# Kernel tuning notes

Hardware: AMD Instinct MI355X
Metric: run time of the kernel (lower is better)

Reference implementation:

```python
import jax, jax.numpy as jnp
import numpy as np

C = 256
CK = C // 8  # query/key projection dim

def conv1x1(x, w, b):
    # x: (B,C,H,W), w: (O,C), b: (O,)
    return jnp.einsum('bchw,oc->bohw', x, w) + b[None, :, None, None]

def conv3x3(x, w, b):
    # w: (O,C,3,3)
    y = jax.lax.conv_general_dilated(x, w, window_strides=(1, 1), padding='SAME',
                                     dimension_numbers=('NCHW', 'OIHW', 'NCHW'))
    return y + b[None, :, None, None]

def setup_inputs() -> dict:
    key = jax.random.key(0)
    ks = jax.random.split(key, 24)
    s = 0.05
    d = {
        'x1': jax.random.normal(ks[0], (4, C, 64, 64), jnp.float32),
        'x2': jax.random.normal(ks[1], (4, C, 64, 64), jnp.float32),
        'wq1': jax.random.normal(ks[2], (CK, C), jnp.float32) * s,
        'bq1': jax.random.normal(ks[3], (CK,), jnp.float32) * s,
        'wk1': jax.random.normal(ks[4], (CK, C), jnp.float32) * s,
        'bk1': jax.random.normal(ks[5], (CK,), jnp.float32) * s,
        'wv1': jax.random.normal(ks[6], (C, C), jnp.float32) * s,
        'bv1': jax.random.normal(ks[7], (C,), jnp.float32) * s,
        'wq2': jax.random.normal(ks[8], (CK, C), jnp.float32) * s,
        'bq2': jax.random.normal(ks[9], (CK,), jnp.float32) * s,
        'wk2': jax.random.normal(ks[10], (CK, C), jnp.float32) * s,
        'bk2': jax.random.normal(ks[11], (CK,), jnp.float32) * s,
        'wv2': jax.random.normal(ks[12], (C, C), jnp.float32) * s,
        'bv2': jax.random.normal(ks[13], (C,), jnp.float32) * s,
        'wd1': jax.random.normal(ks[14], (C, C), jnp.float32) * s,
        'bd1': jax.random.normal(ks[15], (C,), jnp.float32) * s,
        'wd3': jax.random.normal(ks[16], (C, C, 3, 3), jnp.float32) * s,
        'bd3': jax.random.normal(ks[17], (C,), jnp.float32) * s,
        'gamma1': jax.random.normal(ks[18], (1,), jnp.float32) * 0.5,
        'gamma2': jax.random.normal(ks[19], (1,), jnp.float32) * 0.5,
    }
    return d

def reference(x1, x2, wq1, bq1, wk1, bk1, wv1, bv1, wq2, bq2, wk2, bk2, wv2, bv2,
              wd1, bd1, wd3, bd3, gamma1, gamma2):
    B, Cc, H, W = x1.shape
    N = H * W
    # projections (1x1 convs), flattened to (B, d, N)
    q1 = conv1x1(x1, wq1, bq1).reshape(B, CK, N)
    k1 = conv1x1(x1, wk1, bk1).reshape(B, CK, N)
    v1 = conv1x1(x1, wv1, bv1).reshape(B, Cc, N)
    q2 = conv1x1(x2, wq2, bq2).reshape(B, CK, N)
    k2 = conv1x1(x2, wk2, bk2).reshape(B, CK, N)
    v2 = conv1x1(x2, wv2, bv2).reshape(B, Cc, N)
    # cross attention 1: queries from x1, keys/values from x2
    energy1 = jnp.einsum('bdi,bdj->bij', q1, k2)          # (B,N,N)
    attn1 = jax.nn.softmax(energy1, axis=-1)
    out1 = jnp.einsum('bcj,bij->bci', v2, attn1).reshape(B, Cc, H, W)
    # cross attention 2: queries from x2, keys/values from x1
    energy2 = jnp.einsum('bdi,bdj->bij', q2, k1)
    attn2 = jax.nn.softmax(energy2, axis=-1)
    out2 = jnp.einsum('bcj,bij->bci', v1, attn2).reshape(B, Cc, H, W)
    # residual conv branches + gamma-scaled skip (norm1/norm2 in source are dead code)
    out1 = out1 + conv1x1(x1, wd1, bd1) + conv3x3(x1, wd3, bd3)
    out2 = out2 + conv1x1(x2, wd1, bd1) + conv3x3(x2, wd3, bd3)
    out1 = x1 + gamma1[0] * out1
    out2 = x2 + gamma2[0] * out2
    return (out1, out2)
```

## Files before the change

### kernel.cpp

```cpp
#include <hip/hip_runtime.h>
#include <hip/hip_bf16.h>

#define CC 256
#define CKD 32
#define NN 4096
#define HH 64
#define WW 64
#define BB 4

#define LOG2E 1.44269504088896f
#define EXPSHIFT 23.0831203874f

typedef __attribute__((ext_vector_type(8))) short short8;
typedef __attribute__((ext_vector_type(4))) float floatx4;

__device__ __forceinline__ unsigned f2bf(float f) {
  union { float f; unsigned u; } v; v.f = f;
  unsigned r = v.u + 0x7fffu + ((v.u >> 16) & 1u);
  return r >> 16;
}
__device__ __forceinline__ float fast_exp2(float x) {
#if __has_builtin(__builtin_amdgcn_exp2f)
  return __builtin_amdgcn_exp2f(x);
#else
  return __expf(x * 0.693147181f);
#endif
}
__device__ __forceinline__ float bf_lo(unsigned u) { return __uint_as_float(u << 16); }
__device__ __forceinline__ float bf_hi(unsigned u) { return __uint_as_float(u & 0xffff0000u); }

__device__ __forceinline__ void bar_lds() {
  asm volatile("s_waitcnt lgkmcnt(0)" ::: "memory");
  __builtin_amdgcn_s_barrier();
}

__global__ __launch_bounds__(256) void xpack_kernel(
    const float* __restrict__ x1, const float* __restrict__ x2,
    unsigned short* __restrict__ Xp) {
  const int t = threadIdx.x;
  const int nb = blockIdx.x, cbk = blockIdx.y, img = blockIdx.z;
  const float* X = ((img >> 2) ? x2 : x1) + (size_t)(img & 3) * CC * NN;
  const int n0 = nb * 64, c0 = cbk * 64;
  __shared__ float tile[64][65];
  const int nl = t & 63, cl0 = t >> 6;
#pragma unroll
  for (int i = 0; i < 16; ++i)
    tile[cl0 + i * 4][nl] = X[(size_t)(c0 + cl0 + i * 4) * NN + n0 + nl];
  __syncthreads();
#pragma unroll
  for (int it = 0; it < 2; ++it) {
    int id = it * 256 + t;
    int nl2 = id >> 3, cc = id & 7;
    short8 v;
#pragma unroll
    for (int j = 0; j < 8; ++j) v[j] = (short)f2bf(tile[cc * 8 + j][nl2]);
    *(short8*)(Xp + (size_t)img * NN * CC + (size_t)(n0 + nl2) * CC + c0 + cc * 8) = v;
  }
}

__global__ __launch_bounds__(256) void wpack_kernel(
    const float* __restrict__ wd1, const float* __restrict__ wd3,
    const float* __restrict__ wq1, const float* __restrict__ wk1,
    const float* __restrict__ wv1,
    const float* __restrict__ wq2, const float* __restrict__ wk2,
    const float* __restrict__ wv2,
    const float* __restrict__ bq1, const float* __restrict__ bk1,
    const float* __restrict__ bv1,
    const float* __restrict__ bq2, const float* __restrict__ bk2,
    const float* __restrict__ bv2,
    unsigned short* __restrict__ Wp, unsigned short* __restrict__ Wqkv,
    float* __restrict__ Bias) {
  const int id = blockIdx.x * 256 + threadIdx.x;
#pragma unroll
  for (int tap = 0; tap < 10; ++tap) {
    float v = (tap < 9) ? wd3[(size_t)id * 9 + tap] : wd1[id];
    Wp[(size_t)tap * (CC * CC) + id] = (unsigned short)f2bf(v);
  }
#pragma unroll
  for (int j = 0; j < 3; ++j) {
    int e = id + j * 65536;
    if (e < 2 * 320 * 256) {
      int inp = e / (320 * 256), rem = e % (320 * 256);
      int o = rem >> 8, c = rem & 255;
      float v;
      if (inp == 0)
        v = (o < 32) ? wq1[o * 256 + c] * LOG2E
            : (o < 64) ? wk1[(o - 32) * 256 + c] : wv1[(o - 64) * 256 + c];
      else
        v = (o < 32) ? wq2[o * 256 + c] * LOG2E
            : (o < 64) ? wk2[(o - 32) * 256 + c] : wv2[(o - 64) * 256 + c];
      Wqkv[e] = (unsigned short)f2bf(v);
    }
  }
  if (id < 640) {
    int inp = id / 320, o = id % 320;
    float v;
    if (inp == 0) v = (o < 32) ? bq1[o] * LOG2E
                      : (o < 64) ? bk1[o - 32] : bv1[o - 64];
    else          v = (o < 32) ? bq2[o] * LOG2E
                      : (o < 64) ? bk2[o - 32] : bv2[o - 64];
    Bias[id] = v;
  }
}

__global__ __launch_bounds__(256) void proj_mfma_kernel(
    const unsigned short* __restrict__ Xp, const unsigned short* __restrict__ Wqkv,
    const float* __restrict__ Bias,
    unsigned short* __restrict__ Qp1, unsigned short* __restrict__ Kp1,
    unsigned short* __restrict__ Vp1,
    unsigned short* __restrict__ Qp2, unsigned short* __restrict__ Kp2,
    unsigned short* __restrict__ Vp2) {
  const int t = threadIdx.x;
  const int w = t >> 6, lane = t & 63;
  const int l15 = lane & 15, g = lane >> 4;
  const int img = blockIdx.x, pb = blockIdx.y;
  const int pix0 = pb * 64;
  const int inp = img >> 2, b = img & 3;
  const unsigned short* Xi = Xp + (size_t)img * NN * CC;
  const unsigned short* Wb = Wqkv + (size_t)inp * 320 * CC;
  const float* Bi = Bias + inp * 320;
  unsigned short* Qp = (inp ? Qp2 : Qp1) + (size_t)b * NN * CKD;
  unsigned short* Kp = (inp ? Kp2 : Kp1) + (size_t)b * NN * CKD;
  unsigned short* Vp = (inp ? Vp2 : Vp1) + (size_t)b * NN * CC;

  __shared__ unsigned short tile[320][72];

  floatx4 acc[4][5];
#pragma unroll
  for (int mf = 0; mf < 4; ++mf)
#pragma unroll
    for (int nf = 0; nf < 5; ++nf) acc[mf][nf] = (floatx4){0.f, 0.f, 0.f, 0.f};
  const int o0w = w * 80;

#pragma unroll
  for (int cb = 0; cb < 8; ++cb) {
    short8 a[4], bfr[5];
#pragma unroll
    for (int mf = 0; mf < 4; ++mf)
      a[mf] = *(const short8*)(Xi + (size_t)(pix0 + mf * 16 + l15) * CC + cb * 32 + g * 8);
#pragma unroll
    for (int nf = 0; nf < 5; ++nf)
      bfr[nf] = *(const short8*)(Wb + (size_t)(o0w + nf * 16 + l15) * CC + cb * 32 + g * 8);
#pragma unroll
    for (int nf = 0; nf < 5; ++nf)
#pragma unroll
      for (int mf = 0; mf < 4; ++mf)
        acc[mf][nf] = __builtin_amdgcn_mfma_f32_16x16x32_bf16(
            a[mf], bfr[nf], acc[mf][nf], 0, 0, 0);
  }

#pragma unroll
  for (int nf = 0; nf < 5; ++nf) {
    float bs = Bi[o0w + nf * 16 + l15];
#pragma unroll
    for (int mf = 0; mf < 4; ++mf) {
      uint2 pk;
      pk.x = f2bf(acc[mf][nf][0] + bs) | (f2bf(acc[mf][nf][1] + bs) << 16);
      pk.y = f2bf(acc[mf][nf][2] + bs) | (f2bf(acc[mf][nf][3] + bs) << 16);
      *(uint2*)&tile[o0w + nf * 16 + l15][mf * 16 + g * 4] = pk;
    }
  }
  __syncthreads();

  {
    const int pix = t >> 2, ch = t & 3;
    short8 vq, vk;
#pragma unroll
    for (int e = 0; e < 8; ++e) {
      vq[e] = (short)tile[ch * 8 + e][pix];
      vk[e] = (short)tile[32 + ch * 8 + e][pix];
    }
    *(short8*)(Qp + (size_t)(pix0 + pix) * CKD + ch * 8) = vq;
    *(short8*)(Kp + (size_t)(pix0 + pix) * CKD + ch * 8) = vk;
  }
#pragma unroll
  for (int it = 0; it < 8; ++it) {
    short8 vv = *(const short8*)&tile[64 + t][it * 8];
    *(short8*)(Vp + ((size_t)((pix0 >> 3) + it) * CC + t) * 8) = vv;
  }
}

__global__ __launch_bounds__(256, 2) void attn_kernel(
    const unsigned short* __restrict__ Qp1, const unsigned short* __restrict__ Kp1,
    const unsigned short* __restrict__ Qp2, const unsigned short* __restrict__ Kp2,
    const unsigned short* __restrict__ Vp1, const unsigned short* __restrict__ Vp2,
    const unsigned short* __restrict__ Xp, const unsigned short* __restrict__ Wp,
    const float* __restrict__ bd1, const float* __restrict__ bd3,
    const float* __restrict__ x1, const float* __restrict__ x2,
    const float* __restrict__ g1, const float* __restrict__ g2,
    float* __restrict__ out) {
  const int t = threadIdx.x;
  const int w = t >> 6, lane = t & 63;
  const int l15 = lane & 15, g = lane >> 4;
  const int att = blockIdx.x, b = blockIdx.y;
  const int yblk = blockIdx.z;
  const int i0 = yblk * 64;

  const unsigned short *Qp, *Kp, *Vp; const float *x; float gamma; float* o;
  if (att == 0) { Qp = Qp1; Kp = Kp2; Vp = Vp2; x = x1; gamma = g1[0]; o = out; }
  else          { Qp = Qp2; Kp = Kp1; Vp = Vp1; x = x2; gamma = g2[0];
                  o = out + (size_t)BB * CC * NN; }
  Qp += (size_t)b * NN * CKD; Kp += (size_t)b * NN * CKD; Vp += (size_t)b * NN * CC;
  x += (size_t)b * CC * NN; o += (size_t)b * CC * NN;
  const unsigned short* Xi = Xp + (size_t)(att * 4 + b) * NN * CC;

  __shared__ union {
    unsigned short ps[4][64][72];
    unsigned short xs[3][66][72];
  } u;
  __shared__ float l_s[64];

  short8 bq = *(const short8*)(Qp + (size_t)(i0 + w * 16 + l15) * CKD + g * 8);

  floatx4 acc[4][4];
#pragma unroll
  for (int a = 0; a < 4; ++a)
#pragma unroll
    for (int c = 0; c < 4; ++c) acc[a][c] = (floatx4){0.f, 0.f, 0.f, 0.f};
  float l_acc = 0.f;
  const floatx4 zinit = {-EXPSHIFT, -EXPSHIFT, -EXPSHIFT, -EXPSHIFT};

  short8 kr[2][4], vr[2][8];
  auto LOADK = [&](int tt, short8* d) {
    const unsigned short* kb = Kp + ((size_t)tt * 64 + l15) * CKD + g * 8;
#pragma unroll
    for (int js = 0; js < 4; ++js) d[js] = *(const short8*)(kb + js * 16 * CKD);
  };
  auto LOADV = [&](int tt, short8* d) {
#pragma unroll
    for (int ks = 0; ks < 2; ++ks)
#pragma unroll
      for (int cs = 0; cs < 4; ++cs)
        d[ks * 4 + cs] = *(const short8*)(Vp +
            (((size_t)tt * 8 + ks * 4 + g) * CC + (w * 64 + cs * 16 + l15)) * 8);
  };
  auto GEMM1 = [&](const short8* kb, unsigned short (*psb)[72]) {
#pragma unroll
    for (int js = 0; js < 4; ++js) {
      floatx4 s = __builtin_amdgcn_mfma_f32_16x16x32_bf16(kb[js], bq, zinit, 0, 0, 0);
      float p0 = fast_exp2(s[0]);
      float p1 = fast_exp2(s[1]);
      float p2 = fast_exp2(s[2]);
      float p3 = fast_exp2(s[3]);
      l_acc += (p0 + p1) + (p2 + p3);
      unsigned u0 = __float_as_uint(p0) + 0x8000u;
      unsigned u1 = __float_as_uint(p1) + 0x8000u;
      unsigned u2 = __float_as_uint(p2) + 0x8000u;
      unsigned u3 = __float_as_uint(p3) + 0x8000u;
      uint2 pk;
      pk.x = __builtin_amdgcn_perm(u1, u0, 0x07060302u);
      pk.y = __builtin_amdgcn_perm(u3, u2, 0x07060302u);
      *(uint2*)&psb[w * 16 + l15][js * 16 + g * 4] = pk;
    }
  };
  auto GEMM2 = [&](const short8* vb, unsigned short (*psb)[72]) {
#pragma unroll
    for (int ks = 0; ks < 2; ++ks) {
      short8 ap[4];
#pragma unroll
      for (int isub = 0; isub < 4; ++isub)
        ap[isub] = *(const short8*)&psb[isub * 16 + l15][ks * 32 + g * 8];
#pragma unroll
      for (int cs = 0; cs < 4; ++cs)
#pragma unroll
        for (int isub = 0; isub < 4; ++isub)
          acc[isub][cs] = __builtin_amdgcn_mfma_f32_16x16x32_bf16(
              ap[isub], vb[ks * 4 + cs], acc[isub][cs], 0, 0, 0);
    }
  };

  LOADK(0, kr[0]); LOADK(1, kr[1]);
  LOADV(0, vr[0]); LOADV(1, vr[1]);
  GEMM1(kr[0], u.ps[0]);
  GEMM1(kr[1], u.ps[1]);
  LOADK(2, kr[0]); LOADK(3, kr[1]);
  bar_lds();

  for (int jt = 0; jt < 64; jt += 2) {
    if (jt + 2 < 64) {
      GEMM1(kr[0], u.ps[(jt + 2) & 3]);
      if (jt + 4 < 64) LOADK(jt + 4, kr[0]);
    }
    GEMM2(vr[0], u.ps[jt & 3]);
    if (jt + 2 < 64) LOADV(jt + 2, vr[0]);
    if (jt + 3 < 64) {
      GEMM1(kr[1], u.ps[(jt + 3) & 3]);
      if (jt + 5 < 64) LOADK(jt + 5, kr[1]);
    }
    GEMM2(vr[1], u.ps[(jt + 1) & 3]);
    if (jt + 3 < 64) LOADV(jt + 3, vr[1]);
    if (jt + 2 < 64) bar_lds();
  }

  l_acc += __shfl_xor(l_acc, 16);
  l_acc += __shfl_xor(l_acc, 32);
  if (g == 0) l_s[w * 16 + l15] = l_acc;
  bar_lds();

#pragma unroll
  for (int isub = 0; isub < 4; ++isub) {
    float linv[4];
#pragma unroll
    for (int r = 0; r < 4; ++r) linv[r] = 1.f / l_s[isub * 16 + g * 4 + r];
#pragma unroll
    for (int cs = 0; cs < 4; ++cs)
#pragma unroll
      for (int r = 0; r < 4; ++r) acc[isub][cs][r] *= linv[r];
  }

  for (int cb = 0; cb < 4; ++cb) {
    const int c0 = cb * 64;
    if (cb) bar_lds();
#pragma unroll
    for (int it = 0; it < 7; ++it) {
      int id = it * 256 + t;
      if (id < 1584) {
        int r = id / 528, rem = id % 528;
        int col = rem >> 3, cc = rem & 7;
        int y = yblk - 1 + r, xx = col - 1;
        short8 v = {0, 0, 0, 0, 0, 0, 0, 0};
        if (y >= 0 && y < HH && xx >= 0 && xx < WW)
          v = *(const short8*)(Xi + (size_t)(y * WW + xx) * CC + c0 + cc * 8);
        *(short8*)&u.xs[r][col][cc * 8] = v;
      }
    }
    bar_lds();
#pragma unroll
    for (int tap = 0; tap < 10; ++tap) {
      const int dy = (tap < 9) ? tap / 3 - 1 : 0;
      const int dx = (tap < 9) ? tap % 3 - 1 : 0;
      const unsigned short* wrow =
          Wp + ((size_t)tap * CC + w * 64 + l15) * CC + c0 + g * 8;
#pragma unroll
      for (int ks = 0; ks < 2; ++ks) {
        short8 af[4], bw[4];
#pragma unroll
        for (int pm = 0; pm < 4; ++pm)
          af[pm] = *(const short8*)&u.xs[1 + dy][1 + pm * 16 + l15 + dx][ks * 32 + g * 8];
#pragma unroll
        for (int on = 0; on < 4; ++on)
          bw[on] = *(const short8*)(wrow + (size_t)(on * 16) * CC + ks * 32);
#pragma unroll
        for (int pm = 0; pm < 4; ++pm)
#pragma unroll
          for (int on = 0; on < 4; ++on)
            acc[pm][on] = __builtin_amdgcn_mfma_f32_16x16x32_bf16(
                af[pm], bw[on], acc[pm][on], 0, 0, 0);
      }
    }
  }

#pragma unroll
  for (int isub = 0; isub < 4; ++isub) {
#pragma unroll
    for (int cs = 0; cs < 4; ++cs) {
      int c = w * 64 + cs * 16 + l15;
      float bs = bd1[c] + bd3[c];
      size_t base = (size_t)c * NN + i0 + isub * 16 + g * 4;
      float4 xr = *(const float4*)(x + base);
      float4 ov;
      ov.x = xr.x + gamma * (acc[isub][cs][0] + bs);
      ov.y = xr.y + gamma * (acc[isub][cs][1] + bs);
      ov.z = xr.z + gamma * (acc[isub][cs][2] + bs);
      ov.w = xr.w + gamma * (acc[isub][cs][3] + bs);
      *(float4*)(o + base) = ov;
    }
  }
}

extern "C" void kernel_launch(void* const* d_in, const int* in_sizes, int n_in,
                              void* d_out, int out_size, void* d_ws, size_t ws_size,
                              hipStream_t stream) {
  const float* x1  = (const float*)d_in[0];
  const float* x2  = (const float*)d_in[1];
  const float* wq1 = (const float*)d_in[2];
  const float* bq1 = (const float*)d_in[3];
  const float* wk1 = (const float*)d_in[4];
  const float* bk1 = (const float*)d_in[5];
  const float* wv1 = (const float*)d_in[6];
  const float* bv1 = (const float*)d_in[7];
  const float* wq2 = (const float*)d_in[8];
  const float* bq2 = (const float*)d_in[9];
  const float* wk2 = (const float*)d_in[10];
  const float* bk2 = (const float*)d_in[11];
  const float* wv2 = (const float*)d_in[12];
  const float* bv2 = (const float*)d_in[13];
  const float* wd1 = (const float*)d_in[14];
  const float* bd1 = (const float*)d_in[15];
  const float* wd3 = (const float*)d_in[16];
  const float* bd3 = (const float*)d_in[17];
  const float* g1  = (const float*)d_in[18];
  const float* g2  = (const float*)d_in[19];
  float* out = (float*)d_out;

  const size_t QB = (size_t)BB * NN * CKD * 2;
  const size_t VB = (size_t)BB * NN * CC * 2;
  const size_t XB = (size_t)2 * BB * NN * CC * 2;
  const size_t WPB = (size_t)10 * CC * CC * 2;
  const size_t WQB = (size_t)2 * 320 * CC * 2;
  char* base = (char*)d_ws;
  unsigned short* Qp1 = (unsigned short*)(base);
  unsigned short* Kp1 = (unsigned short*)(base + QB);
  unsigned short* Qp2 = (unsigned short*)(base + 2 * QB);
  unsigned short* Kp2 = (unsigned short*)(base + 3 * QB);
  unsigned short* Vp1 = (unsigned short*)(base + 4 * QB);
  unsigned short* Vp2 = (unsigned short*)(base + 4 * QB + VB);
  unsigned short* Xp  = (unsigned short*)(base + 4 * QB + 2 * VB);
  unsigned short* Wp  = (unsigned short*)(base + 4 * QB + 2 * VB + XB);
  unsigned short* Wqkv = (unsigned short*)(base + 4 * QB + 2 * VB + XB + WPB);
  float* Bias = (float*)(base + 4 * QB + 2 * VB + XB + WPB + WQB);

  xpack_kernel<<<dim3(NN / 64, CC / 64, 2 * BB), 256, 0, stream>>>(x1, x2, Xp);
  wpack_kernel<<<dim3(CC * CC / 256), 256, 0, stream>>>(
      wd1, wd3, wq1, wk1, wv1, wq2, wk2, wv2,
      bq1, bk1, bv1, bq2, bk2, bv2, Wp, Wqkv, Bias);

  proj_mfma_kernel<<<dim3(2 * BB, NN / 64), 256, 0, stream>>>(
      Xp, Wqkv, Bias, Qp1, Kp1, Vp1, Qp2, Kp2, Vp2);

  attn_kernel<<<dim3(2, BB, NN / 64), 256, 0, stream>>>(
      Qp1, Kp1, Qp2, Kp2, Vp1, Vp2, Xp, Wp, bd1, bd3, x1, x2, g1, g2, out);
}
```

Before: 296.8 us.

## Merge pack kernels and hoist P-tile LDS reads ahead of GEMM1 in attention loop

Merges the activation-pack and weight-pack kernels into one launch, using the extra z-slice of the grid for the weight conversion, which removes one kernel launch. In the attention main loop, the P fragments for both pending GEMM2 steps are now read from LDS at the top of each iteration, before GEMM1 runs, so the LDS latency overlaps MFMA work. The GEMM2 MFMAs are also wrapped in s_setprio raises. The cost is higher register pressure from holding 16 extra short8 fragments, which could reduce occupancy or cause spills.

```diff
diff --git a/kernel.cpp b/kernel.cpp
--- a/kernel.cpp
+++ b/kernel.cpp
@@ -34,31 +34,9 @@
   __builtin_amdgcn_s_barrier();
 }
 
-__global__ __launch_bounds__(256) void xpack_kernel(
+__global__ __launch_bounds__(256) void pack_kernel(
     const float* __restrict__ x1, const float* __restrict__ x2,
-    unsigned short* __restrict__ Xp) {
-  const int t = threadIdx.x;
-  const int nb = blockIdx.x, cbk = blockIdx.y, img = blockIdx.z;
-  const float* X = ((img >> 2) ? x2 : x1) + (size_t)(img & 3) * CC * NN;
-  const int n0 = nb * 64, c0 = cbk * 64;
-  __shared__ float tile[64][65];
-  const int nl = t & 63, cl0 = t >> 6;
-#pragma unroll
-  for (int i = 0; i < 16; ++i)
-    tile[cl0 + i * 4][nl] = X[(size_t)(c0 + cl0 + i * 4) * NN + n0 + nl];
-  __syncthreads();
-#pragma unroll
-  for (int it = 0; it < 2; ++it) {
-    int id = it * 256 + t;
-    int nl2 = id >> 3, cc = id & 7;
-    short8 v;
-#pragma unroll
-    for (int j = 0; j < 8; ++j) v[j] = (short)f2bf(tile[cc * 8 + j][nl2]);
-    *(short8*)(Xp + (size_t)img * NN * CC + (size_t)(n0 + nl2) * CC + c0 + cc * 8) = v;
-  }
-}
-
-__global__ __launch_bounds__(256) void wpack_kernel(
+    unsigned short* __restrict__ Xp,
     const float* __restrict__ wd1, const float* __restrict__ wd3,
     const float* __restrict__ wq1, const float* __restrict__ wk1,
     const float* __restrict__ wv1,
@@ -70,36 +48,58 @@
     const float* __restrict__ bv2,
     unsigned short* __restrict__ Wp, unsigned short* __restrict__ Wqkv,
     float* __restrict__ Bias) {
-  const int id = blockIdx.x * 256 + threadIdx.x;
-#pragma unroll
-  for (int tap = 0; tap < 10; ++tap) {
-    float v = (tap < 9) ? wd3[(size_t)id * 9 + tap] : wd1[id];
-    Wp[(size_t)tap * (CC * CC) + id] = (unsigned short)f2bf(v);
-  }
-#pragma unroll
-  for (int j = 0; j < 3; ++j) {
-    int e = id + j * 65536;
-    if (e < 2 * 320 * 256) {
-      int inp = e / (320 * 256), rem = e % (320 * 256);
-      int o = rem >> 8, c = rem & 255;
+  const int t = threadIdx.x;
+  __shared__ float tile[64][65];
+  if (blockIdx.z < 8) {
+    const int nb = blockIdx.x, cbk = blockIdx.y, img = blockIdx.z;
+    const float* X = ((img >> 2) ? x2 : x1) + (size_t)(img & 3) * CC * NN;
+    const int n0 = nb * 64, c0 = cbk * 64;
+    const int nl = t & 63, cl0 = t >> 6;
+#pragma unroll
+    for (int i = 0; i < 16; ++i)
+      tile[cl0 + i * 4][nl] = X[(size_t)(c0 + cl0 + i * 4) * NN + n0 + nl];
+    __syncthreads();
+#pragma unroll
+    for (int it = 0; it < 2; ++it) {
+      int id = it * 256 + t;
+      int nl2 = id >> 3, cc = id & 7;
+      short8 v;
+#pragma unroll
+      for (int j = 0; j < 8; ++j) v[j] = (short)f2bf(tile[cc * 8 + j][nl2]);
+      *(short8*)(Xp + (size_t)img * NN * CC + (size_t)(n0 + nl2) * CC + c0 + cc * 8) = v;
+    }
+  } else {
+    const int id = (blockIdx.y * 64 + blockIdx.x) * 256 + t;
+#pragma unroll
+    for (int tap = 0; tap < 10; ++tap) {
+      float v = (tap < 9) ? wd3[(size_t)id * 9 + tap] : wd1[id];
+      Wp[(size_t)tap * (CC * CC) + id] = (unsigned short)f2bf(v);
+    }
+#pragma unroll
+    for (int j = 0; j < 3; ++j) {
+      int e = id + j * 65536;
+      if (e < 2 * 320 * 256) {
+        int inp = e / (320 * 256), rem = e % (320 * 256);
+        int o = rem >> 8, c = rem & 255;
+        float v;
+        if (inp == 0)
+          v = (o < 32) ? wq1[o * 256 + c] * LOG2E
+              : (o < 64) ? wk1[(o - 32) * 256 + c] : wv1[(o - 64) * 256 + c];
+        else
+          v = (o < 32) ? wq2[o * 256 + c] * LOG2E
+              : (o < 64) ? wk2[(o - 32) * 256 + c] : wv2[(o - 64) * 256 + c];
+        Wqkv[e] = (unsigned short)f2bf(v);
+      }
+    }
+    if (id < 640) {
+      int inp = id / 320, o = id % 320;
       float v;
-      if (inp == 0)
-        v = (o < 32) ? wq1[o * 256 + c] * LOG2E
-            : (o < 64) ? wk1[(o - 32) * 256 + c] : wv1[(o - 64) * 256 + c];
-      else
-        v = (o < 32) ? wq2[o * 256 + c] * LOG2E
-            : (o < 64) ? wk2[(o - 32) * 256 + c] : wv2[(o - 64) * 256 + c];
-      Wqkv[e] = (unsigned short)f2bf(v);
-    }
-  }
-  if (id < 640) {
-    int inp = id / 320, o = id % 320;
-    float v;
-    if (inp == 0) v = (o < 32) ? bq1[o] * LOG2E
-                      : (o < 64) ? bk1[o - 32] : bv1[o - 64];
-    else          v = (o < 32) ? bq2[o] * LOG2E
-                      : (o < 64) ? bk2[o - 32] : bv2[o - 64];
-    Bias[id] = v;
+      if (inp == 0) v = (o < 32) ? bq1[o] * LOG2E
+                        : (o < 64) ? bk1[o - 32] : bv1[o - 64];
+      else          v = (o < 32) ? bq2[o] * LOG2E
+                        : (o < 64) ? bk2[o - 32] : bv2[o - 64];
+      Bias[id] = v;
+    }
   }
 }
 
@@ -253,20 +253,17 @@
       *(uint2*)&psb[w * 16 + l15][js * 16 + g * 4] = pk;
     }
   };
-  auto GEMM2 = [&](const short8* vb, unsigned short (*psb)[72]) {
-#pragma unroll
-    for (int ks = 0; ks < 2; ++ks) {
-      short8 ap[4];
-#pragma unroll
-      for (int isub = 0; isub < 4; ++isub)
-        ap[isub] = *(const short8*)&psb[isub * 16 + l15][ks * 32 + g * 8];
+  auto GEMM2R = [&](const short8* vb, const short8* pa_) {
+    __builtin_amdgcn_s_setprio(1);
+#pragma unroll
+    for (int ks = 0; ks < 2; ++ks)
 #pragma unroll
       for (int cs = 0; cs < 4; ++cs)
 #pragma unroll
         for (int isub = 0; isub < 4; ++isub)
           acc[isub][cs] = __builtin_amdgcn_mfma_f32_16x16x32_bf16(
-              ap[isub], vb[ks * 4 + cs], acc[isub][cs], 0, 0, 0);
-    }
+              pa_[ks * 4 + isub], vb[ks * 4 + cs], acc[isub][cs], 0, 0, 0);
+    __builtin_amdgcn_s_setprio(0);
   };
 
   LOADK(0, kr[0]); LOADK(1, kr[1]);
@@ -277,17 +274,27 @@
   bar_lds();
 
   for (int jt = 0; jt < 64; jt += 2) {
+    short8 pa0[8], pa1[8];
+#pragma unroll
+    for (int ks = 0; ks < 2; ++ks)
+#pragma unroll
+      for (int isub = 0; isub < 4; ++isub) {
+        pa0[ks * 4 + isub] =
+            *(const short8*)&u.ps[jt & 3][isub * 16 + l15][ks * 32 + g * 8];
+        pa1[ks * 4 + isub] =
+            *(const short8*)&u.ps[(jt + 1) & 3][isub * 16 + l15][ks * 32 + g * 8];
+      }
     if (jt + 2 < 64) {
       GEMM1(kr[0], u.ps[(jt + 2) & 3]);
       if (jt + 4 < 64) LOADK(jt + 4, kr[0]);
     }
-    GEMM2(vr[0], u.ps[jt & 3]);
+    GEMM2R(vr[0], pa0);
     if (jt + 2 < 64) LOADV(jt + 2, vr[0]);
     if (jt + 3 < 64) {
       GEMM1(kr[1], u.ps[(jt + 3) & 3]);
       if (jt + 5 < 64) LOADK(jt + 5, kr[1]);
     }
-    GEMM2(vr[1], u.ps[(jt + 1) & 3]);
+    GEMM2R(vr[1], pa1);
     if (jt + 3 < 64) LOADV(jt + 3, vr[1]);
     if (jt + 2 < 64) bar_lds();
   }
@@ -410,9 +417,8 @@
   unsigned short* Wqkv = (unsigned short*)(base + 4 * QB + 2 * VB + XB + WPB);
   float* Bias = (float*)(base + 4 * QB + 2 * VB + XB + WPB + WQB);
 
-  xpack_kernel<<<dim3(NN / 64, CC / 64, 2 * BB), 256, 0, stream>>>(x1, x2, Xp);
-  wpack_kernel<<<dim3(CC * CC / 256), 256, 0, stream>>>(
-      wd1, wd3, wq1, wk1, wv1, wq2, wk2, wv2,
+  pack_kernel<<<dim3(NN / 64, CC / 64, 9), 256, 0, stream>>>(
+      x1, x2, Xp, wd1, wd3, wq1, wk1, wv1, wq2, wk2, wv2,
       bq1, bk1, bv1, bq2, bk2, bv2, Wp, Wqkv, Bias);
 
   proj_mfma_kernel<<<dim3(2 * BB, NN / 64), 256, 0, stream>>>(
```

Result: slower. 318.1 us (+7.2%).
